# Kernel tuning notes

Hardware: AMD Instinct MI355X
Metric: run time of the kernel (lower is better)

## Reference

```python
import jax, jax.numpy as jnp
import numpy as np

N = 8192          # total genes
B = 16            # number of ragged batch groups (equal-size here: 512 each)
D = 768           # hidden_dim
NEG = -1.0e9      # mask fill value used by the original module


def setup_inputs() -> dict:
    key = jax.random.key(0)
    ks = jax.random.split(key, 10)
    s = 0.02
    inp = {
        "gene_embeddings": jax.random.normal(ks[0], (N, D), dtype=jnp.float32),
        # sorted group ids: 16 contiguous groups of 512 genes
        "batch": (jnp.arange(N) // (N // B)).astype(jnp.int64),
        "Wq": jax.random.normal(ks[1], (D, D), dtype=jnp.float32) * s,
        "bq": jnp.zeros((D,), dtype=jnp.float32),
        "Wk": jax.random.normal(ks[2], (D, D), dtype=jnp.float32) * s,
        "bk": jnp.zeros((D,), dtype=jnp.float32),
        "Wv": jax.random.normal(ks[3], (D, D), dtype=jnp.float32) * s,
        "bv": jnp.zeros((D,), dtype=jnp.float32),
        "Wo": jax.random.normal(ks[4], (D, D), dtype=jnp.float32) * s,
        "bo": jnp.zeros((D,), dtype=jnp.float32),
        "beta": jnp.ones((1,), dtype=jnp.float32) * 0.1,
    }
    return inp


def reference(gene_embeddings, batch, Wq, bq, Wk, bk, Wv, bv, Wo, bo, beta):
    # Single-head attention over full hidden_dim (num_heads unused in original).
    x = gene_embeddings
    q = x @ Wq.T + bq                      # [N, D]
    k = x @ Wk.T + bk
    v = x @ Wv.T + bv
    scale = 1.0 / jnp.sqrt(jnp.asarray(D, dtype=x.dtype))
    scores = (q @ k.T) * scale             # [N, N]
    # block-diagonal group mask + diagonal self-mask (same -1e9 fill as torch code)
    same_group = batch[:, None] == batch[None, :]
    eye = jnp.eye(N, dtype=bool)
    allow = same_group & (~eye)
    scores = jnp.where(allow, scores, NEG)
    weights = jax.nn.softmax(scores, axis=-1)   # dropout in eval mode -> identity
    dyn = weights @ v                       # [N, D]
    dyn = dyn @ Wo.T + bo
    return x + beta * dyn
```

## Files before the change

### kernel.cpp

```cpp
#include <hip/hip_runtime.h>
#include <hip/hip_bf16.h>
#include <cstdint>

using u16 = unsigned short;
using u32 = unsigned int;

typedef __bf16 bf16x8 __attribute__((ext_vector_type(8)));
typedef float  f32x4  __attribute__((ext_vector_type(4)));

__device__ __forceinline__ u32 f2b2(float a, float b) {
    __hip_bfloat162 h = __float22bfloat162_rn(float2{a, b});
    u32 u;
    __builtin_memcpy(&u, &h, 4);
    return u;
}
__device__ __forceinline__ float b2f(u16 b) {
    u32 u = (u32)b << 16;
    float f;
    __builtin_memcpy(&f, &u, 4);
    return f;
}

__device__ __forceinline__ void gload_lds16(const u16* g, u16* l) {
    __builtin_amdgcn_global_load_lds(
        (const __attribute__((address_space(1))) void*)g,
        (__attribute__((address_space(3))) void*)l,
        16, 0, 0);
}

__launch_bounds__(256)
__global__ void pack_kernel(const float* __restrict__ x,
                            const float* __restrict__ Wq,
                            const float* __restrict__ Wk,
                            const float* __restrict__ Wv,
                            const float* __restrict__ Wo,
                            const float* __restrict__ bq,
                            const float* __restrict__ bv,
                            const float* __restrict__ bo,
                            u16* __restrict__ xb,
                            u16* __restrict__ Wob,
                            u16* __restrict__ WqT,
                            u16* __restrict__ WkT,
                            u16* __restrict__ WvT,
                            float* __restrict__ czk,
                            float* __restrict__ bvoo)
{
    __shared__ u16 tl[64][72];
    const int b = blockIdx.x, tid = threadIdx.x;

    if (b < 3360) {
        int c = b * 256 + tid;
        long e = (long)c * 8;
        const float* src; u16* dst; long off;
        if (e < 6291456L) { src = x;  dst = xb;  off = e; }
        else              { src = Wo; dst = Wob; off = e - 6291456L; }
        float4 v0 = *(const float4*)(src + off);
        float4 v1 = *(const float4*)(src + off + 4);
        uint4 o;
        o.x = f2b2(v0.x, v0.y); o.y = f2b2(v0.z, v0.w);
        o.z = f2b2(v1.x, v1.y); o.w = f2b2(v1.z, v1.w);
        *(uint4*)(dst + off) = o;
    } else if (b < 3792) {
        int t = b - 3360;
        int w = t / 144, tt = t % 144;
        int tr = tt / 12, tc = tt % 12;
        const float* src0 = (w == 0) ? Wq : (w == 1) ? Wk : Wv;
        u16* dst0 = (w == 0) ? WqT : (w == 1) ? WkT : WvT;
        int lr = tid >> 2, lcb = (tid & 3) * 16;
        const float* src = src0 + (long)(tr * 64 + lr) * 768 + tc * 64 + lcb;
#pragma unroll
        for (int q = 0; q < 4; q++) {
            float4 v = *(const float4*)(src + q * 4);
            u32 p0 = f2b2(v.x, v.y), p1 = f2b2(v.z, v.w);
            tl[lr][lcb + q * 4 + 0] = (u16)p0;
            tl[lr][lcb + q * 4 + 1] = (u16)(p0 >> 16);
            tl[lr][lcb + q * 4 + 2] = (u16)p1;
            tl[lr][lcb + q * 4 + 3] = (u16)(p1 >> 16);
        }
        __syncthreads();
        int li = tid >> 2, lkb = (tid & 3) * 16;
        u16 o[16];
#pragma unroll
        for (int j = 0; j < 16; j++) o[j] = tl[lkb + j][li];
        u16* dst = dst0 + (long)(tc * 64 + li) * 768 + tr * 64 + lkb;
#pragma unroll
        for (int j = 0; j < 16; j++) dst[j] = o[j];
    } else if (b < 3984) {
        int wave = tid >> 6, lane = tid & 63;
        int j = (b - 3792) * 4 + wave;
        float acc = 0.f;
#pragma unroll
        for (int i = 0; i < 12; i++) {
            int rr = i * 64 + lane;
            acc += Wk[(long)rr * 768 + j] * bq[rr];
        }
#pragma unroll
        for (int d = 32; d; d >>= 1) acc += __shfl_xor(acc, d);
        if (lane == 0) czk[j] = acc;
    } else {
        int wave = tid >> 6, lane = tid & 63;
        int j = (b - 3984) * 4 + wave;
        float acc = 0.f;
#pragma unroll
        for (int i = 0; i < 12; i++) {
            int k = i * 64 + lane;
            acc += Wo[(long)j * 768 + k] * bv[k];
        }
#pragma unroll
        for (int d = 32; d; d >>= 1) acc += __shfl_xor(acc, d);
        if (lane == 0) bvoo[j] = acc + bo[j];
    }
}

template<int TM, int TN, int MODE>
__device__ __forceinline__ void gemm_body(
        const u16* __restrict__ A, int lda, long sAz,
        const u16* __restrict__ B, int ldb, long sBz,
        void* __restrict__ Cv, int ldc, long sCz,
        int K,
        const float* __restrict__ bias,
        float scale,
        u16* __restrict__ vTout)
{
    constexpr int FI = TM / 32;
    constexpr int FJ = TN / 32;
    constexpr int CA = TM / 64;
    constexpr int CB = TN / 64;

    __shared__ u16 As[2][TM * 32];
    __shared__ u16 Bs[2][TN * 32];

    const int tid  = threadIdx.x;
    const int g    = blockIdx.z;
    const u16* Ab = A + (long)g * sAz + (long)blockIdx.y * TM * lda;
    const u16* Bb = B + (long)g * sBz + (long)blockIdx.x * TN * ldb;

    const int wave = tid >> 6, lane = tid & 63;
    const int wm = (wave >> 1) * (TM / 2), wn = (wave & 1) * (TN / 2);
    const int ln15 = lane & 15, lq = lane >> 4;

    f32x4 acc[FI][FJ];
#pragma unroll
    for (int i = 0; i < FI; i++)
#pragma unroll
        for (int j = 0; j < FJ; j++)
            acc[i][j] = (f32x4){0.f, 0.f, 0.f, 0.f};

    const int srow = lane >> 2;
    const int sc   = ((lane & 3) ^ ((lane >> 4) & 3)) * 8;
    const u16* Ag[CA]; const u16* Bg[CB];
    int Al[CA], Bl[CB];
#pragma unroll
    for (int t = 0; t < CA; t++) {
        int c = wave * CA + t;
        Ag[t] = Ab + (long)(c * 16 + srow) * lda + sc;
        Al[t] = c * 512;
    }
#pragma unroll
    for (int t = 0; t < CB; t++) {
        int c = wave * CB + t;
        Bg[t] = Bb + (long)(c * 16 + srow) * ldb + sc;
        Bl[t] = c * 512;
    }

    const int foff = ln15 * 32 + ((lq ^ (ln15 >> 2)) * 8);
    const int nk = K >> 5;

#pragma unroll
    for (int t = 0; t < CA; t++) gload_lds16(Ag[t], &As[0][Al[t]]);
#pragma unroll
    for (int t = 0; t < CB; t++) gload_lds16(Bg[t], &Bs[0][Bl[t]]);

    for (int kt = 0; kt < nk; kt++) {
        const int cur = kt & 1;
        __syncthreads();
        if (kt + 1 < nk) {
            const int k0 = (kt + 1) * 32, nxt = cur ^ 1;
#pragma unroll
            for (int t = 0; t < CA; t++) gload_lds16(Ag[t] + k0, &As[nxt][Al[t]]);
#pragma unroll
            for (int t = 0; t < CB; t++) gload_lds16(Bg[t] + k0, &Bs[nxt][Bl[t]]);
        }

        bf16x8 af[FI], bfr[FJ];
#pragma unroll
        for (int i = 0; i < FI; i++)
            af[i] = *(const bf16x8*)&As[cur][(wm / 16 + i) * 512 + foff];
#pragma unroll
        for (int j = 0; j < FJ; j++)
            bfr[j] = *(const bf16x8*)&Bs[cur][(wn / 16 + j) * 512 + foff];
#pragma unroll
        for (int i = 0; i < FI; i++)
#pragma unroll
            for (int j = 0; j < FJ; j++)
                acc[i][j] = __builtin_amdgcn_mfma_f32_16x16x32_bf16(af[i], bfr[j], acc[i][j], 0, 0, 0);
    }

    const int baseRow = blockIdx.y * TM + wm;
    const int baseCol = blockIdx.x * TN + wn;

    if constexpr (MODE == 0) {
        if (baseCol < 768) {
            u16* C = (u16*)Cv;
#pragma unroll
            for (int i = 0; i < FI; i++)
#pragma unroll
                for (int j = 0; j < FJ; j++) {
                    int col = baseCol + j * 16 + ln15;
                    float bb = bias[col];
                    u32 p01 = f2b2(acc[i][j][0] + bb, acc[i][j][1] + bb);
                    u32 p23 = f2b2(acc[i][j][2] + bb, acc[i][j][3] + bb);
                    long r0 = (long)(baseRow + i * 16 + lq * 4) * ldc + col;
                    C[r0]           = (u16)p01;
                    C[r0 + ldc]     = (u16)(p01 >> 16);
                    C[r0 + 2 * ldc] = (u16)p23;
                    C[r0 + 3 * ldc] = (u16)(p23 >> 16);
                }
        } else {
#pragma unroll
            for (int i = 0; i < FI; i++)
#pragma unroll
                for (int j = 0; j < FJ; j++) {
                    int col = baseCol + j * 16 + ln15;
                    uint2 o;
                    o.x = f2b2(acc[i][j][0], acc[i][j][1]);
                    o.y = f2b2(acc[i][j][2], acc[i][j][3]);
                    *(uint2*)(vTout + (long)(col - 768) * 8192
                              + baseRow + i * 16 + lq * 4) = o;
                }
        }
    } else {
        u16* C = (u16*)Cv + (long)g * sCz;
#pragma unroll
        for (int i = 0; i < FI; i++)
#pragma unroll
            for (int j = 0; j < FJ; j++) {
                int col = baseCol + j * 16 + ln15;
                u32 p01 = f2b2(acc[i][j][0], acc[i][j][1]);
                u32 p23 = f2b2(acc[i][j][2], acc[i][j][3]);
                long r0 = (long)(baseRow + i * 16 + lq * 4) * ldc + col;
                C[r0]           = (u16)p01;
                C[r0 + ldc]     = (u16)(p01 >> 16);
                C[r0 + 2 * ldc] = (u16)p23;
                C[r0 + 3 * ldc] = (u16)(p23 >> 16);
            }
    }
}

__launch_bounds__(256)
__global__ void k_ww(const u16* WA, const u16* WB, void* WZplus)
{
    gemm_body<64, 128, 3>(WA, 768, 589824L, WB, 768, 589824L,
                          WZplus, 768, -589824L, 768,
                          nullptr, 0.f, nullptr);
}
__launch_bounds__(256)
__global__ void k_zv(const u16* A, const u16* B, void* C, const float* bias,
                     u16* vTout)
{
    gemm_body<128, 128, 0>(A, 768, 0, B, 768, 0, C, 768, 0, 768,
                           bias, 0.f, vTout);
}

__launch_bounds__(512)
__global__ void k_fattn(const u16* __restrict__ zbuf,
                        const u16* __restrict__ xb,
                        const u16* __restrict__ vwT,
                        float* __restrict__ out,
                        const float* __restrict__ bvoo,
                        const float* __restrict__ betaPtr,
                        float scale)
{
    __shared__ __align__(16) u16 smem[57344];
    u16* zl = smem;
    u16* xB = smem + 24576;
    u16* Pl = smem;
    u16* Vs = smem + 16384;

    const int rt = blockIdx.x, g = blockIdx.y;
    const int tid = threadIdx.x;
    const int wave = tid >> 6, lane = tid & 63;
    const int ln15 = lane & 15, lq = lane >> 4;
    const int srow = lane >> 2;
    const int sc   = ((lane & 3) ^ ((lane >> 4) & 3)) * 8;
    const int foff = ln15 * 32 + ((lq ^ (ln15 >> 2)) * 8);

    const long rowBase = (long)(g * 512 + rt * 32);
    const u16* Zb = zbuf + rowBase * 768;
    const u16* Xg = xb + (long)g * 512 * 768;

    const int wm = (wave >> 2) * 16;
    const int wn = (wave & 3) * 128;

#pragma unroll
    for (int n = 0; n < 6; n++) {
        int cc = n * 8 + wave;
        int zkt = cc >> 1, c = cc & 1;
        gload_lds16(Zb + (long)(c * 16 + srow) * 768 + zkt * 32 + sc,
                    &zl[cc * 512]);
    }
    const u16* Bg[4]; int Bl[4];
#pragma unroll
    for (int t = 0; t < 4; t++) {
        int c = wave * 4 + t;
        Bg[t] = Xg + (long)(c * 16 + srow) * 768 + sc;
        Bl[t] = c * 512;
    }
#pragma unroll
    for (int t = 0; t < 4; t++) gload_lds16(Bg[t], &xB[Bl[t]]);

    f32x4 acc[8];
#pragma unroll
    for (int j = 0; j < 8; j++) acc[j] = (f32x4){0.f, 0.f, 0.f, 0.f};

    for (int kt = 0; kt < 24; kt++) {
        const int cur = kt & 1;
        __syncthreads();
        if (kt + 1 < 24) {
            const int k0 = (kt + 1) * 32, nxt = cur ^ 1;
#pragma unroll
            for (int t = 0; t < 4; t++)
                gload_lds16(Bg[t] + k0, &xB[nxt * 16384 + Bl[t]]);
        }
        bf16x8 af = *(const bf16x8*)&zl[(kt * 2 + (wm >> 4)) * 512 + foff];
        bf16x8 bfr[8];
#pragma unroll
        for (int j = 0; j < 8; j++)
            bfr[j] = *(const bf16x8*)&xB[cur * 16384 + (wn / 16 + j) * 512 + foff];
#pragma unroll
        for (int j = 0; j < 8; j++)
            acc[j] = __builtin_amdgcn_mfma_f32_16x16x32_bf16(af, bfr[j], acc[j], 0, 0, 0);
    }

    __syncthreads();

#pragma unroll
    for (int sub = 0; sub < 2; sub++)
        gload_lds16(vwT + (long)(wave * 16 + srow) * 8192 + g * 512 + sub * 32 + sc,
                    &Vs[sub * 4096 + wave * 512]);

#pragma unroll
    for (int j = 0; j < 8; j++) {
        int col = wn + j * 16 + ln15;
        int c8 = col >> 3, b7 = col & 7;
#pragma unroll
        for (int r = 0; r < 4; r++) {
            int row = wm + lq * 4 + r;
            float v = acc[j][r] * scale;
            if (rt * 32 + row == col) v = -1.0e9f;
            Pl[(row * 64 + (c8 ^ (row & 7))) * 8 + b7] = (u16)f2b2(v, v);
        }
    }
    __syncthreads();

    {
        const int r = tid >> 4, seg = tid & 15;
        float e[32];
        float m = -3.0e38f;
#pragma unroll
        for (int q = 0; q < 4; q++) {
            int c8 = seg * 4 + q;
            uint4 qv = *(const uint4*)&Pl[(r * 64 + (c8 ^ (r & 7))) * 8];
            u32 w[4] = {qv.x, qv.y, qv.z, qv.w};
#pragma unroll
            for (int h = 0; h < 4; h++) {
                float lo = b2f((u16)w[h]);
                float hi = b2f((u16)(w[h] >> 16));
                e[q * 8 + h * 2]     = lo;
                e[q * 8 + h * 2 + 1] = hi;
                m = fmaxf(m, fmaxf(lo, hi));
            }
        }
        m = fmaxf(m, __shfl_xor(m, 1));
        m = fmaxf(m, __shfl_xor(m, 2));
        m = fmaxf(m, __shfl_xor(m, 4));
        m = fmaxf(m, __shfl_xor(m, 8));
        float sum = 0.f;
#pragma unroll
        for (int jj = 0; jj < 32; jj++) { e[jj] = __expf(e[jj] - m); sum += e[jj]; }
        sum += __shfl_xor(sum, 1);
        sum += __shfl_xor(sum, 2);
        sum += __shfl_xor(sum, 4);
        sum += __shfl_xor(sum, 8);
        const float inv = 1.0f / sum;
#pragma unroll
        for (int q = 0; q < 4; q++) {
            int c8 = seg * 4 + q;
            uint4 o;
            o.x = f2b2(e[q * 8 + 0] * inv, e[q * 8 + 1] * inv);
            o.y = f2b2(e[q * 8 + 2] * inv, e[q * 8 + 3] * inv);
            o.z = f2b2(e[q * 8 + 4] * inv, e[q * 8 + 5] * inv);
            o.w = f2b2(e[q * 8 + 6] * inv, e[q * 8 + 7] * inv);
            *(uint4*)&Pl[(r * 64 + (c8 ^ (r & 7))) * 8] = o;
        }
    }
    __syncthreads();

    const int wnP = (wave & 3) * 32;
    const int prow = wm + ln15;
    const float bet = betaPtr[0];

    bf16x8 apr[16];
#pragma unroll
    for (int k4 = 0; k4 < 16; k4++)
        apr[k4] = *(const bf16x8*)&Pl[(prow * 64 + ((k4 * 4 + lq) ^ (prow & 7))) * 8];

    f32x4 accP[2];
    accP[0] = (f32x4){0.f, 0.f, 0.f, 0.f};
    accP[1] = (f32x4){0.f, 0.f, 0.f, 0.f};

    for (int ct = 0; ct < 6; ct++) {
#pragma unroll
        for (int k8 = 0; k8 < 8; k8++) {
            const int t = ct * 8 + k8;
            const int cur = t & 1;
            __syncthreads();
            if (t + 1 < 48) {
                const int tn = t + 1, ctn = tn >> 3, kn = tn & 7;
#pragma unroll
                for (int sub = 0; sub < 2; sub++)
                    gload_lds16(vwT + (long)(ctn * 128 + wave * 16 + srow) * 8192
                                    + g * 512 + kn * 64 + sub * 32 + sc,
                                &Vs[(cur ^ 1) * 8192 + sub * 4096 + wave * 512]);
            }
#pragma unroll
            for (int sub = 0; sub < 2; sub++) {
                const int kt = k8 * 2 + sub;
                bf16x8 b0 = *(const bf16x8*)&Vs[cur * 8192 + sub * 4096
                                                + (wnP >> 4) * 512 + foff];
                bf16x8 b1 = *(const bf16x8*)&Vs[cur * 8192 + sub * 4096
                                                + ((wnP >> 4) + 1) * 512 + foff];
                accP[0] = __builtin_amdgcn_mfma_f32_16x16x32_bf16(apr[kt], b0, accP[0], 0, 0, 0);
                accP[1] = __builtin_amdgcn_mfma_f32_16x16x32_bf16(apr[kt], b1, accP[1], 0, 0, 0);
            }
        }
        {
            const u16* Xr = xb + (rowBase + wm + lq * 4) * 768;
            float* O = out + (rowBase + wm + lq * 4) * 768;
#pragma unroll
            for (int j = 0; j < 2; j++) {
                const int col = ct * 128 + wnP + j * 16 + ln15;
                const float bb = bvoo[col];
#pragma unroll
                for (int rr = 0; rr < 4; rr++)
                    O[rr * 768 + col] = b2f(Xr[rr * 768 + col])
                                        + bet * (accP[j][rr] + bb);
                accP[j] = (f32x4){0.f, 0.f, 0.f, 0.f};
            }
        }
    }
}

extern "C" void kernel_launch(void* const* d_in, const int* in_sizes, int n_in,
                              void* d_out, int out_size, void* d_ws, size_t ws_size,
                              hipStream_t stream)
{
    const float* x    = (const float*)d_in[0];
    const float* Wq   = (const float*)d_in[2];
    const float* bq   = (const float*)d_in[3];
    const float* Wk   = (const float*)d_in[4];
    const float* bk   = (const float*)d_in[5];
    const float* Wv   = (const float*)d_in[6];
    const float* bv   = (const float*)d_in[7];
    const float* Wo   = (const float*)d_in[8];
    const float* bo   = (const float*)d_in[9];
    const float* beta = (const float*)d_in[10];
    float* out = (float*)d_out;
    (void)bk;

    char* ws = (char*)d_ws;
    u16*   zbuf = (u16*)(ws + 0);
    u16*   vwT  = (u16*)(ws + 12582912);
    u16*   xb   = (u16*)(ws + 25165824);
    u16*   WA   = (u16*)(ws + 46137344);
    u16*   WB   = (u16*)(ws + 48496640);
    u16*   WZ   = (u16*)(ws + 50855936);
    float* czk  = (float*)(ws + 53215232);
    float* bvoo = (float*)(ws + 53218304);

    u16* Wob = WA;
    u16* WkT = WA + 589824;
    u16* WvT = WB;
    u16* WqT = WB + 589824;

    const float scale = 0.03608439182435161f;

    pack_kernel<<<4176, 256, 0, stream>>>(x, Wq, Wk, Wv, Wo, bq, bv, bo,
                                          xb, Wob, WqT, WkT, WvT, czk, bvoo);

    k_ww<<<dim3(6, 12, 2), 256, 0, stream>>>(WA, WB, (void*)(WZ + 589824L));

    k_zv<<<dim3(12, 64, 1), 256, 0, stream>>>(xb, WZ, (void*)zbuf, czk, vwT);

    k_fattn<<<dim3(16, 16), 512, 0, stream>>>(zbuf, xb, vwT, out, bvoo, beta,
                                              scale);
}
```

Before: 203.6 us.

## Restructure fused attention kernel with register-staged prefetch and in-register softmax

Rewrites the fused attention kernel's S=ZX^T stage so each wave owns a column strip, and prefetches the X tiles through registers several k-steps ahead instead of using async global-to-LDS loads with a barrier every step. Softmax now runs directly on the MFMA accumulators with cross-wave max/sum reductions through small LDS buffers. Normalisation is deferred to the output epilogue. The PV stage drops its per-step __syncthreads by giving each wave a private V slice in LDS, and blocks are remapped to a 1D grid with launch_bounds(512,2). These changes target barrier stalls and LDS round-trips, at the cost of more register pressure and a risk of LDS write/read hazards without barriers.

```diff
diff --git a/kernel.cpp b/kernel.cpp
--- a/kernel.cpp
+++ b/kernel.cpp
@@ -262,7 +262,7 @@
                            bias, 0.f, vTout);
 }
 
-__launch_bounds__(512)
+__launch_bounds__(512, 2)
 __global__ void k_fattn(const u16* __restrict__ zbuf,
                         const u16* __restrict__ xb,
                         const u16* __restrict__ vwT,
@@ -275,178 +275,251 @@
     u16* zl = smem;
     u16* xB = smem + 24576;
     u16* Pl = smem;
-    u16* Vs = smem + 16384;
-
-    const int rt = blockIdx.x, g = blockIdx.y;
+    float* redM = (float*)(smem + 16640);
+    float* redS = (float*)(smem + 16640 + 512);
+    u16* Vs = smem + 24576;
+
+    const int bx = blockIdx.x;
+    const int lg = ((bx & 7) << 5) + (bx >> 3);
+    const int g = lg >> 4, rt = lg & 15;
+
     const int tid = threadIdx.x;
     const int wave = tid >> 6, lane = tid & 63;
     const int ln15 = lane & 15, lq = lane >> 4;
     const int srow = lane >> 2;
-    const int sc   = ((lane & 3) ^ ((lane >> 4) & 3)) * 8;
+    const int sc = ((lane & 3) ^ ((lane >> 4) & 3)) * 8;
     const int foff = ln15 * 32 + ((lq ^ (ln15 >> 2)) * 8);
 
     const long rowBase = (long)(g * 512 + rt * 32);
     const u16* Zb = zbuf + rowBase * 768;
     const u16* Xg = xb + (long)g * 512 * 768;
 
-    const int wm = (wave >> 2) * 16;
-    const int wn = (wave & 3) * 128;
-
 #pragma unroll
     for (int n = 0; n < 6; n++) {
         int cc = n * 8 + wave;
-        int zkt = cc >> 1, c = cc & 1;
-        gload_lds16(Zb + (long)(c * 16 + srow) * 768 + zkt * 32 + sc,
+        gload_lds16(Zb + (long)((cc & 1) * 16 + srow) * 768 + (cc >> 1) * 32 + sc,
                     &zl[cc * 512]);
     }
-    const u16* Bg[4]; int Bl[4];
+    const u16* xsrc[4];
+    u16* xd[4];
 #pragma unroll
     for (int t = 0; t < 4; t++) {
-        int c = wave * 4 + t;
-        Bg[t] = Xg + (long)(c * 16 + srow) * 768 + sc;
-        Bl[t] = c * 512;
-    }
-#pragma unroll
-    for (int t = 0; t < 4; t++) gload_lds16(Bg[t], &xB[Bl[t]]);
-
-    f32x4 acc[8];
-#pragma unroll
-    for (int j = 0; j < 8; j++) acc[j] = (f32x4){0.f, 0.f, 0.f, 0.f};
-
-    for (int kt = 0; kt < 24; kt++) {
-        const int cur = kt & 1;
-        __syncthreads();
-        if (kt + 1 < 24) {
-            const int k0 = (kt + 1) * 32, nxt = cur ^ 1;
-#pragma unroll
-            for (int t = 0; t < 4; t++)
-                gload_lds16(Bg[t] + k0, &xB[nxt * 16384 + Bl[t]]);
-        }
-        bf16x8 af = *(const bf16x8*)&zl[(kt * 2 + (wm >> 4)) * 512 + foff];
-        bf16x8 bfr[8];
-#pragma unroll
-        for (int j = 0; j < 8; j++)
-            bfr[j] = *(const bf16x8*)&xB[cur * 16384 + (wn / 16 + j) * 512 + foff];
-#pragma unroll
-        for (int j = 0; j < 8; j++)
-            acc[j] = __builtin_amdgcn_mfma_f32_16x16x32_bf16(af, bfr[j], acc[j], 0, 0, 0);
-    }
-
+        xsrc[t] = Xg + (long)((wave * 4 + t) * 16 + srow) * 768 + sc;
+        xd[t] = xB + (wave * 4 + t) * 512 + lane * 8;
+    }
+    uint4 vrA[4], vrB[4];
+#pragma unroll
+    for (int t = 0; t < 4; t++) vrA[t] = *(const uint4*)(xsrc[t]);
+#pragma unroll
+    for (int t = 0; t < 4; t++) *(uint4*)(xd[t]) = vrA[t];
+#pragma unroll
+    for (int t = 0; t < 4; t++) vrA[t] = *(const uint4*)(xsrc[t] + 32);
+#pragma unroll
+    for (int t = 0; t < 4; t++) vrB[t] = *(const uint4*)(xsrc[t] + 64);
     __syncthreads();
 
-#pragma unroll
-    for (int sub = 0; sub < 2; sub++)
-        gload_lds16(vwT + (long)(wave * 16 + srow) * 8192 + g * 512 + sub * 32 + sc,
-                    &Vs[sub * 4096 + wave * 512]);
-
-#pragma unroll
-    for (int j = 0; j < 8; j++) {
-        int col = wn + j * 16 + ln15;
-        int c8 = col >> 3, b7 = col & 7;
-#pragma unroll
-        for (int r = 0; r < 4; r++) {
-            int row = wm + lq * 4 + r;
-            float v = acc[j][r] * scale;
-            if (rt * 32 + row == col) v = -1.0e9f;
-            Pl[(row * 64 + (c8 ^ (row & 7))) * 8 + b7] = (u16)f2b2(v, v);
-        }
+    f32x4 acc0[4], acc1[4];
+#pragma unroll
+    for (int j = 0; j < 4; j++) {
+        acc0[j] = (f32x4){0.f, 0.f, 0.f, 0.f};
+        acc1[j] = (f32x4){0.f, 0.f, 0.f, 0.f};
+    }
+
+    for (int kt2 = 0; kt2 < 12; kt2++) {
+        const int ke = kt2 * 2;
+        {
+#pragma unroll
+            for (int t = 0; t < 4; t++) *(uint4*)(xd[t] + 16384) = vrA[t];
+            int kl = ke + 3; if (kl > 23) kl = 23;
+#pragma unroll
+            for (int t = 0; t < 4; t++) vrA[t] = *(const uint4*)(xsrc[t] + kl * 32);
+            bf16x8 af0 = *(const bf16x8*)&zl[(ke * 2 + 0) * 512 + foff];
+            bf16x8 af1 = *(const bf16x8*)&zl[(ke * 2 + 1) * 512 + foff];
+#pragma unroll
+            for (int j = 0; j < 4; j++) {
+                bf16x8 bfr = *(const bf16x8*)&xB[(wave * 4 + j) * 512 + foff];
+                acc0[j] = __builtin_amdgcn_mfma_f32_16x16x32_bf16(af0, bfr, acc0[j], 0, 0, 0);
+                acc1[j] = __builtin_amdgcn_mfma_f32_16x16x32_bf16(af1, bfr, acc1[j], 0, 0, 0);
+            }
+        }
+        {
+            const int ko = ke + 1;
+#pragma unroll
+            for (int t = 0; t < 4; t++) *(uint4*)(xd[t]) = vrB[t];
+            int kl = ko + 3; if (kl > 23) kl = 23;
+#pragma unroll
+            for (int t = 0; t < 4; t++) vrB[t] = *(const uint4*)(xsrc[t] + kl * 32);
+            bf16x8 af0 = *(const bf16x8*)&zl[(ko * 2 + 0) * 512 + foff];
+            bf16x8 af1 = *(const bf16x8*)&zl[(ko * 2 + 1) * 512 + foff];
+#pragma unroll
+            for (int j = 0; j < 4; j++) {
+                bf16x8 bfr = *(const bf16x8*)&xB[16384 + (wave * 4 + j) * 512 + foff];
+                acc0[j] = __builtin_amdgcn_mfma_f32_16x16x32_bf16(af0, bfr, acc0[j], 0, 0, 0);
+                acc1[j] = __builtin_amdgcn_mfma_f32_16x16x32_bf16(af1, bfr, acc1[j], 0, 0, 0);
+            }
+        }
+    }
+
+    const int wm3 = (wave >> 2) * 16;
+    const int wn3 = (wave & 3) * 32;
+    const u16* vbase[4];
+    u16* vdst[4];
+#pragma unroll
+    for (int scj = 0; scj < 4; scj++) {
+        vbase[scj] = vwT + (long)(wn3 + (scj & 1) * 16 + srow) * 8192
+                     + g * 512 + (scj >> 1) * 32 + sc;
+        vdst[scj] = Vs + wave * 2048 + scj * 512 + lane * 8;
+    }
+    uint4 w0[4], w1[4];
+#pragma unroll
+    for (int scj = 0; scj < 4; scj++) {
+        w0[scj] = *(const uint4*)(vbase[scj]);
+        w1[scj] = *(const uint4*)(vbase[scj] + 64);
     }
     __syncthreads();
 
-    {
-        const int r = tid >> 4, seg = tid & 15;
-        float e[32];
-        float m = -3.0e38f;
-#pragma unroll
-        for (int q = 0; q < 4; q++) {
-            int c8 = seg * 4 + q;
-            uint4 qv = *(const uint4*)&Pl[(r * 64 + (c8 ^ (r & 7))) * 8];
-            u32 w[4] = {qv.x, qv.y, qv.z, qv.w};
-#pragma unroll
-            for (int h = 0; h < 4; h++) {
-                float lo = b2f((u16)w[h]);
-                float hi = b2f((u16)(w[h] >> 16));
-                e[q * 8 + h * 2]     = lo;
-                e[q * 8 + h * 2 + 1] = hi;
-                m = fmaxf(m, fmaxf(lo, hi));
-            }
-        }
-        m = fmaxf(m, __shfl_xor(m, 1));
-        m = fmaxf(m, __shfl_xor(m, 2));
-        m = fmaxf(m, __shfl_xor(m, 4));
-        m = fmaxf(m, __shfl_xor(m, 8));
-        float sum = 0.f;
-#pragma unroll
-        for (int jj = 0; jj < 32; jj++) { e[jj] = __expf(e[jj] - m); sum += e[jj]; }
-        sum += __shfl_xor(sum, 1);
-        sum += __shfl_xor(sum, 2);
-        sum += __shfl_xor(sum, 4);
-        sum += __shfl_xor(sum, 8);
-        const float inv = 1.0f / sum;
-#pragma unroll
-        for (int q = 0; q < 4; q++) {
-            int c8 = seg * 4 + q;
-            uint4 o;
-            o.x = f2b2(e[q * 8 + 0] * inv, e[q * 8 + 1] * inv);
-            o.y = f2b2(e[q * 8 + 2] * inv, e[q * 8 + 3] * inv);
-            o.z = f2b2(e[q * 8 + 4] * inv, e[q * 8 + 5] * inv);
-            o.w = f2b2(e[q * 8 + 6] * inv, e[q * 8 + 7] * inv);
-            *(uint4*)&Pl[(r * 64 + (c8 ^ (r & 7))) * 8] = o;
+    float e0[4][4], e1[4][4], mx0[4], mx1[4];
+#pragma unroll
+    for (int rr = 0; rr < 4; rr++) { mx0[rr] = -3.0e38f; mx1[rr] = -3.0e38f; }
+#pragma unroll
+    for (int j = 0; j < 4; j++)
+#pragma unroll
+        for (int rr = 0; rr < 4; rr++) {
+            const int col = wave * 64 + j * 16 + ln15;
+            float v0 = acc0[j][rr] * scale;
+            float v1 = acc1[j][rr] * scale;
+            if (rt * 32 + lq * 4 + rr == col) v0 = -1.0e9f;
+            if (rt * 32 + 16 + lq * 4 + rr == col) v1 = -1.0e9f;
+            e0[j][rr] = v0; e1[j][rr] = v1;
+            mx0[rr] = fmaxf(mx0[rr], v0);
+            mx1[rr] = fmaxf(mx1[rr], v1);
+        }
+#pragma unroll
+    for (int rr = 0; rr < 4; rr++)
+#pragma unroll
+        for (int d = 1; d < 16; d <<= 1) {
+            mx0[rr] = fmaxf(mx0[rr], __shfl_xor(mx0[rr], d));
+            mx1[rr] = fmaxf(mx1[rr], __shfl_xor(mx1[rr], d));
+        }
+    if (ln15 == 0) {
+#pragma unroll
+        for (int rr = 0; rr < 4; rr++) {
+            redM[(lq * 4 + rr) * 8 + wave] = mx0[rr];
+            redM[(16 + lq * 4 + rr) * 8 + wave] = mx1[rr];
         }
     }
     __syncthreads();
-
-    const int wnP = (wave & 3) * 32;
-    const int prow = wm + ln15;
+    float m0[4], m1[4], s0[4], s1[4];
+#pragma unroll
+    for (int rr = 0; rr < 4; rr++) {
+        float a = -3.0e38f, b = -3.0e38f;
+#pragma unroll
+        for (int w = 0; w < 8; w++) {
+            a = fmaxf(a, redM[(lq * 4 + rr) * 8 + w]);
+            b = fmaxf(b, redM[(16 + lq * 4 + rr) * 8 + w]);
+        }
+        m0[rr] = a; m1[rr] = b; s0[rr] = 0.f; s1[rr] = 0.f;
+    }
+#pragma unroll
+    for (int j = 0; j < 4; j++)
+#pragma unroll
+        for (int rr = 0; rr < 4; rr++) {
+            e0[j][rr] = __expf(e0[j][rr] - m0[rr]); s0[rr] += e0[j][rr];
+            e1[j][rr] = __expf(e1[j][rr] - m1[rr]); s1[rr] += e1[j][rr];
+        }
+#pragma unroll
+    for (int rr = 0; rr < 4; rr++)
+#pragma unroll
+        for (int d = 1; d < 16; d <<= 1) {
+            s0[rr] += __shfl_xor(s0[rr], d);
+            s1[rr] += __shfl_xor(s1[rr], d);
+        }
+    if (ln15 == 0) {
+#pragma unroll
+        for (int rr = 0; rr < 4; rr++) {
+            redS[(lq * 4 + rr) * 8 + wave] = s0[rr];
+            redS[(16 + lq * 4 + rr) * 8 + wave] = s1[rr];
+        }
+    }
+#pragma unroll
+    for (int j = 0; j < 4; j++)
+#pragma unroll
+        for (int rr = 0; rr < 4; rr++) {
+            const int col = wave * 64 + j * 16 + ln15;
+            Pl[(lq * 4 + rr) * 520 + col] = (u16)f2b2(e0[j][rr], e0[j][rr]);
+            Pl[(16 + lq * 4 + rr) * 520 + col] = (u16)f2b2(e1[j][rr], e1[j][rr]);
+        }
+    __syncthreads();
+
+    float invS[4];
+#pragma unroll
+    for (int rr = 0; rr < 4; rr++) {
+        float s = 0.f;
+#pragma unroll
+        for (int w = 0; w < 8; w++) s += redS[(wm3 + lq * 4 + rr) * 8 + w];
+        invS[rr] = 1.0f / s;
+    }
+    bf16x8 apr[16];
+#pragma unroll
+    for (int k4 = 0; k4 < 16; k4++)
+        apr[k4] = *(const bf16x8*)&Pl[(wm3 + ln15) * 520 + (k4 * 4 + lq) * 8];
+
     const float bet = betaPtr[0];
-
-    bf16x8 apr[16];
-#pragma unroll
-    for (int k4 = 0; k4 < 16; k4++)
-        apr[k4] = *(const bf16x8*)&Pl[(prow * 64 + ((k4 * 4 + lq) ^ (prow & 7))) * 8];
-
-    f32x4 accP[2];
-    accP[0] = (f32x4){0.f, 0.f, 0.f, 0.f};
-    accP[1] = (f32x4){0.f, 0.f, 0.f, 0.f};
+    f32x4 aP0 = (f32x4){0.f, 0.f, 0.f, 0.f};
+    f32x4 aP1 = (f32x4){0.f, 0.f, 0.f, 0.f};
 
     for (int ct = 0; ct < 6; ct++) {
 #pragma unroll
         for (int k8 = 0; k8 < 8; k8++) {
             const int t = ct * 8 + k8;
-            const int cur = t & 1;
-            __syncthreads();
-            if (t + 1 < 48) {
-                const int tn = t + 1, ctn = tn >> 3, kn = tn & 7;
-#pragma unroll
-                for (int sub = 0; sub < 2; sub++)
-                    gload_lds16(vwT + (long)(ctn * 128 + wave * 16 + srow) * 8192
-                                    + g * 512 + kn * 64 + sub * 32 + sc,
-                                &Vs[(cur ^ 1) * 8192 + sub * 4096 + wave * 512]);
+            if ((k8 & 1) == 0) {
+#pragma unroll
+                for (int scj = 0; scj < 4; scj++) *(uint4*)(vdst[scj]) = w0[scj];
+                int tt = t + 2; if (tt > 47) tt = 47;
+                const long off = (long)(tt >> 3) * 1048576 + (tt & 7) * 64;
+#pragma unroll
+                for (int scj = 0; scj < 4; scj++)
+                    w0[scj] = *(const uint4*)(vbase[scj] + off);
+            } else {
+#pragma unroll
+                for (int scj = 0; scj < 4; scj++) *(uint4*)(vdst[scj]) = w1[scj];
+                int tt = t + 2; if (tt > 47) tt = 47;
+                const long off = (long)(tt >> 3) * 1048576 + (tt & 7) * 64;
+#pragma unroll
+                for (int scj = 0; scj < 4; scj++)
+                    w1[scj] = *(const uint4*)(vbase[scj] + off);
             }
-#pragma unroll
-            for (int sub = 0; sub < 2; sub++) {
-                const int kt = k8 * 2 + sub;
-                bf16x8 b0 = *(const bf16x8*)&Vs[cur * 8192 + sub * 4096
-                                                + (wnP >> 4) * 512 + foff];
-                bf16x8 b1 = *(const bf16x8*)&Vs[cur * 8192 + sub * 4096
-                                                + ((wnP >> 4) + 1) * 512 + foff];
-                accP[0] = __builtin_amdgcn_mfma_f32_16x16x32_bf16(apr[kt], b0, accP[0], 0, 0, 0);
-                accP[1] = __builtin_amdgcn_mfma_f32_16x16x32_bf16(apr[kt], b1, accP[1], 0, 0, 0);
-            }
+            __builtin_amdgcn_sched_barrier(0);
+            bf16x8 b00 = *(const bf16x8*)&Vs[wave * 2048 + 0 * 512 + foff];
+            bf16x8 b01 = *(const bf16x8*)&Vs[wave * 2048 + 1 * 512 + foff];
+            bf16x8 b10 = *(const bf16x8*)&Vs[wave * 2048 + 2 * 512 + foff];
+            bf16x8 b11 = *(const bf16x8*)&Vs[wave * 2048 + 3 * 512 + foff];
+            aP0 = __builtin_amdgcn_mfma_f32_16x16x32_bf16(apr[k8 * 2 + 0], b00, aP0, 0, 0, 0);
+            aP1 = __builtin_amdgcn_mfma_f32_16x16x32_bf16(apr[k8 * 2 + 0], b01, aP1, 0, 0, 0);
+            aP0 = __builtin_amdgcn_mfma_f32_16x16x32_bf16(apr[k8 * 2 + 1], b10, aP0, 0, 0, 0);
+            aP1 = __builtin_amdgcn_mfma_f32_16x16x32_bf16(apr[k8 * 2 + 1], b11, aP1, 0, 0, 0);
         }
         {
-            const u16* Xr = xb + (rowBase + wm + lq * 4) * 768;
-            float* O = out + (rowBase + wm + lq * 4) * 768;
-#pragma unroll
-            for (int j = 0; j < 2; j++) {
-                const int col = ct * 128 + wnP + j * 16 + ln15;
+            const u16* Xr = xb + (rowBase + wm3 + lq * 4) * 768;
+            float* O = out + (rowBase + wm3 + lq * 4) * 768;
+            {
+                const int col = ct * 128 + wn3 + ln15;
                 const float bb = bvoo[col];
 #pragma unroll
                 for (int rr = 0; rr < 4; rr++)
                     O[rr * 768 + col] = b2f(Xr[rr * 768 + col])
-                                        + bet * (accP[j][rr] + bb);
-                accP[j] = (f32x4){0.f, 0.f, 0.f, 0.f};
+                                        + bet * (invS[rr] * aP0[rr] + bb);
             }
+            {
+                const int col = ct * 128 + wn3 + 16 + ln15;
+                const float bb = bvoo[col];
+#pragma unroll
+                for (int rr = 0; rr < 4; rr++)
+                    O[rr * 768 + col] = b2f(Xr[rr * 768 + col])
+                                        + bet * (invS[rr] * aP1[rr] + bb);
+            }
+            aP0 = (f32x4){0.f, 0.f, 0.f, 0.f};
+            aP1 = (f32x4){0.f, 0.f, 0.f, 0.f};
         }
     }
 }
@@ -492,6 +565,6 @@
 
     k_zv<<<dim3(12, 64, 1), 256, 0, stream>>>(xb, WZ, (void*)zbuf, czk, vwT);
 
-    k_fattn<<<dim3(16, 16), 512, 0, stream>>>(zbuf, xb, vwT, out, bvoo, beta,
-                                              scale);
-}
+    k_fattn<<<dim3(256), 512, 0, stream>>>(zbuf, xb, vwT, out, bvoo, beta,
+                                           scale);
+}
```

Result: slower. 301.1 us (+47.9%).

## Compute softmax in registers with cross-wave LDS reduction, deferred normalization, larger V tiles

Applied to the files above, without the earlier changes.

Softmax max and sum are now computed directly on the MFMA accumulators, with shuffles and a small LDS reduction across waves. This removes the separate pass that round-tripped bf16 scores through LDS, and the 1/sum scaling is applied in the output epilogue. The V streaming loop now loads 128-column K chunks, which halves the number of barrier-separated pipeline steps. The grid is flattened to 1D with a swizzled block-to-group mapping, which may change L2 locality. The unnormalized probabilities are rounded to bf16 before normalization, a slight numeric change.

```diff
diff --git a/kernel.cpp b/kernel.cpp
--- a/kernel.cpp
+++ b/kernel.cpp
@@ -275,14 +275,19 @@
     u16* zl = smem;
     u16* xB = smem + 24576;
     u16* Pl = smem;
-    u16* Vs = smem + 16384;
-
-    const int rt = blockIdx.x, g = blockIdx.y;
+    float* redM = (float*)(smem + 16384);
+    float* redS = (float*)(smem + 16640);
+    u16* Vs = smem + 18432;
+
+    const int bx = blockIdx.x;
+    const int lg = ((bx & 7) << 5) + (bx >> 3);
+    const int g = lg >> 4, rt = lg & 15;
+
     const int tid = threadIdx.x;
     const int wave = tid >> 6, lane = tid & 63;
     const int ln15 = lane & 15, lq = lane >> 4;
     const int srow = lane >> 2;
-    const int sc   = ((lane & 3) ^ ((lane >> 4) & 3)) * 8;
+    const int sc = ((lane & 3) ^ ((lane >> 4) & 3)) * 8;
     const int foff = ln15 * 32 + ((lq ^ (ln15 >> 2)) * 8);
 
     const long rowBase = (long)(g * 512 + rt * 32);
@@ -295,8 +300,7 @@
 #pragma unroll
     for (int n = 0; n < 6; n++) {
         int cc = n * 8 + wave;
-        int zkt = cc >> 1, c = cc & 1;
-        gload_lds16(Zb + (long)(c * 16 + srow) * 768 + zkt * 32 + sc,
+        gload_lds16(Zb + (long)((cc & 1) * 16 + srow) * 768 + (cc >> 1) * 32 + sc,
                     &zl[cc * 512]);
     }
     const u16* Bg[4]; int Bl[4];
@@ -335,118 +339,140 @@
     __syncthreads();
 
 #pragma unroll
-    for (int sub = 0; sub < 2; sub++)
+    for (int sub = 0; sub < 4; sub++)
         gload_lds16(vwT + (long)(wave * 16 + srow) * 8192 + g * 512 + sub * 32 + sc,
                     &Vs[sub * 4096 + wave * 512]);
 
+    float mx[4];
+#pragma unroll
+    for (int rr = 0; rr < 4; rr++) mx[rr] = -3.0e38f;
+#pragma unroll
+    for (int j = 0; j < 8; j++)
+#pragma unroll
+        for (int rr = 0; rr < 4; rr++) {
+            const int col = wn + j * 16 + ln15;
+            float v = acc[j][rr] * scale;
+            if (rt * 32 + wm + lq * 4 + rr == col) v = -1.0e9f;
+            acc[j][rr] = v;
+            mx[rr] = fmaxf(mx[rr], v);
+        }
+#pragma unroll
+    for (int rr = 0; rr < 4; rr++) {
+        mx[rr] = fmaxf(mx[rr], __shfl_xor(mx[rr], 1));
+        mx[rr] = fmaxf(mx[rr], __shfl_xor(mx[rr], 2));
+        mx[rr] = fmaxf(mx[rr], __shfl_xor(mx[rr], 4));
+        mx[rr] = fmaxf(mx[rr], __shfl_xor(mx[rr], 8));
+    }
+    if (ln15 == 0) {
+#pragma unroll
+        for (int rr = 0; rr < 4; rr++)
+            redM[(wm + lq * 4 + rr) * 4 + (wave & 3)] = mx[rr];
+    }
+    __syncthreads();
+
+    float m[4], s[4];
+#pragma unroll
+    for (int rr = 0; rr < 4; rr++) {
+        float4 rm = *(const float4*)&redM[(wm + lq * 4 + rr) * 4];
+        m[rr] = fmaxf(fmaxf(rm.x, rm.y), fmaxf(rm.z, rm.w));
+        s[rr] = 0.f;
+    }
+#pragma unroll
+    for (int j = 0; j < 8; j++)
+#pragma unroll
+        for (int rr = 0; rr < 4; rr++) {
+            float p = __expf(acc[j][rr] - m[rr]);
+            acc[j][rr] = p;
+            s[rr] += p;
+        }
+#pragma unroll
+    for (int rr = 0; rr < 4; rr++) {
+        s[rr] += __shfl_xor(s[rr], 1);
+        s[rr] += __shfl_xor(s[rr], 2);
+        s[rr] += __shfl_xor(s[rr], 4);
+        s[rr] += __shfl_xor(s[rr], 8);
+    }
+    if (ln15 == 0) {
+#pragma unroll
+        for (int rr = 0; rr < 4; rr++)
+            redS[(wm + lq * 4 + rr) * 4 + (wave & 3)] = s[rr];
+    }
 #pragma unroll
     for (int j = 0; j < 8; j++) {
-        int col = wn + j * 16 + ln15;
-        int c8 = col >> 3, b7 = col & 7;
-#pragma unroll
-        for (int r = 0; r < 4; r++) {
-            int row = wm + lq * 4 + r;
-            float v = acc[j][r] * scale;
-            if (rt * 32 + row == col) v = -1.0e9f;
-            Pl[(row * 64 + (c8 ^ (row & 7))) * 8 + b7] = (u16)f2b2(v, v);
+        const int col = wn + j * 16 + ln15;
+        const int c8 = col >> 3, b7 = col & 7;
+#pragma unroll
+        for (int rr = 0; rr < 4; rr++) {
+            const int row = wm + lq * 4 + rr;
+            Pl[(row * 64 + (c8 ^ (row & 7))) * 8 + b7] = (u16)f2b2(acc[j][rr], acc[j][rr]);
         }
     }
     __syncthreads();
 
-    {
-        const int r = tid >> 4, seg = tid & 15;
-        float e[32];
-        float m = -3.0e38f;
-#pragma unroll
-        for (int q = 0; q < 4; q++) {
-            int c8 = seg * 4 + q;
-            uint4 qv = *(const uint4*)&Pl[(r * 64 + (c8 ^ (r & 7))) * 8];
-            u32 w[4] = {qv.x, qv.y, qv.z, qv.w};
-#pragma unroll
-            for (int h = 0; h < 4; h++) {
-                float lo = b2f((u16)w[h]);
-                float hi = b2f((u16)(w[h] >> 16));
-                e[q * 8 + h * 2]     = lo;
-                e[q * 8 + h * 2 + 1] = hi;
-                m = fmaxf(m, fmaxf(lo, hi));
-            }
-        }
-        m = fmaxf(m, __shfl_xor(m, 1));
-        m = fmaxf(m, __shfl_xor(m, 2));
-        m = fmaxf(m, __shfl_xor(m, 4));
-        m = fmaxf(m, __shfl_xor(m, 8));
-        float sum = 0.f;
-#pragma unroll
-        for (int jj = 0; jj < 32; jj++) { e[jj] = __expf(e[jj] - m); sum += e[jj]; }
-        sum += __shfl_xor(sum, 1);
-        sum += __shfl_xor(sum, 2);
-        sum += __shfl_xor(sum, 4);
-        sum += __shfl_xor(sum, 8);
-        const float inv = 1.0f / sum;
-#pragma unroll
-        for (int q = 0; q < 4; q++) {
-            int c8 = seg * 4 + q;
-            uint4 o;
-            o.x = f2b2(e[q * 8 + 0] * inv, e[q * 8 + 1] * inv);
-            o.y = f2b2(e[q * 8 + 2] * inv, e[q * 8 + 3] * inv);
-            o.z = f2b2(e[q * 8 + 4] * inv, e[q * 8 + 5] * inv);
-            o.w = f2b2(e[q * 8 + 6] * inv, e[q * 8 + 7] * inv);
-            *(uint4*)&Pl[(r * 64 + (c8 ^ (r & 7))) * 8] = o;
-        }
-    }
-    __syncthreads();
-
-    const int wnP = (wave & 3) * 32;
+    float invS[4];
+#pragma unroll
+    for (int rr = 0; rr < 4; rr++) {
+        float4 rs = *(const float4*)&redS[(wm + lq * 4 + rr) * 4];
+        invS[rr] = 1.0f / (rs.x + rs.y + rs.z + rs.w);
+    }
+
     const int prow = wm + ln15;
-    const float bet = betaPtr[0];
-
     bf16x8 apr[16];
 #pragma unroll
     for (int k4 = 0; k4 < 16; k4++)
         apr[k4] = *(const bf16x8*)&Pl[(prow * 64 + ((k4 * 4 + lq) ^ (prow & 7))) * 8];
 
-    f32x4 accP[2];
-    accP[0] = (f32x4){0.f, 0.f, 0.f, 0.f};
-    accP[1] = (f32x4){0.f, 0.f, 0.f, 0.f};
+    const int wnP = (wave & 3) * 32;
+    const float bet = betaPtr[0];
+    f32x4 aP0 = (f32x4){0.f, 0.f, 0.f, 0.f};
+    f32x4 aP1 = (f32x4){0.f, 0.f, 0.f, 0.f};
 
     for (int ct = 0; ct < 6; ct++) {
 #pragma unroll
-        for (int k8 = 0; k8 < 8; k8++) {
-            const int t = ct * 8 + k8;
-            const int cur = t & 1;
+        for (int kn2 = 0; kn2 < 4; kn2++) {
+            const int ts = ct * 4 + kn2;
+            const int cur = ts & 1;
             __syncthreads();
-            if (t + 1 < 48) {
-                const int tn = t + 1, ctn = tn >> 3, kn = tn & 7;
-#pragma unroll
-                for (int sub = 0; sub < 2; sub++)
+            if (ts + 1 < 24) {
+                const int tn = ts + 1, ctn = tn >> 2, kn = tn & 3;
+                const int nxt = cur ^ 1;
+#pragma unroll
+                for (int sub = 0; sub < 4; sub++)
                     gload_lds16(vwT + (long)(ctn * 128 + wave * 16 + srow) * 8192
-                                    + g * 512 + kn * 64 + sub * 32 + sc,
-                                &Vs[(cur ^ 1) * 8192 + sub * 4096 + wave * 512]);
+                                    + g * 512 + kn * 128 + sub * 32 + sc,
+                                &Vs[nxt * 16384 + sub * 4096 + wave * 512]);
             }
 #pragma unroll
-            for (int sub = 0; sub < 2; sub++) {
-                const int kt = k8 * 2 + sub;
-                bf16x8 b0 = *(const bf16x8*)&Vs[cur * 8192 + sub * 4096
+            for (int sub = 0; sub < 4; sub++) {
+                bf16x8 b0 = *(const bf16x8*)&Vs[cur * 16384 + sub * 4096
                                                 + (wnP >> 4) * 512 + foff];
-                bf16x8 b1 = *(const bf16x8*)&Vs[cur * 8192 + sub * 4096
+                bf16x8 b1 = *(const bf16x8*)&Vs[cur * 16384 + sub * 4096
                                                 + ((wnP >> 4) + 1) * 512 + foff];
-                accP[0] = __builtin_amdgcn_mfma_f32_16x16x32_bf16(apr[kt], b0, accP[0], 0, 0, 0);
-                accP[1] = __builtin_amdgcn_mfma_f32_16x16x32_bf16(apr[kt], b1, accP[1], 0, 0, 0);
+                aP0 = __builtin_amdgcn_mfma_f32_16x16x32_bf16(apr[kn2 * 4 + sub], b0, aP0, 0, 0, 0);
+                aP1 = __builtin_amdgcn_mfma_f32_16x16x32_bf16(apr[kn2 * 4 + sub], b1, aP1, 0, 0, 0);
             }
         }
         {
             const u16* Xr = xb + (rowBase + wm + lq * 4) * 768;
             float* O = out + (rowBase + wm + lq * 4) * 768;
-#pragma unroll
-            for (int j = 0; j < 2; j++) {
-                const int col = ct * 128 + wnP + j * 16 + ln15;
+            {
+                const int col = ct * 128 + wnP + ln15;
                 const float bb = bvoo[col];
 #pragma unroll
                 for (int rr = 0; rr < 4; rr++)
                     O[rr * 768 + col] = b2f(Xr[rr * 768 + col])
-                                        + bet * (accP[j][rr] + bb);
-                accP[j] = (f32x4){0.f, 0.f, 0.f, 0.f};
+                                        + bet * (invS[rr] * aP0[rr] + bb);
             }
+            {
+                const int col = ct * 128 + wnP + 16 + ln15;
+                const float bb = bvoo[col];
+#pragma unroll
+                for (int rr = 0; rr < 4; rr++)
+                    O[rr * 768 + col] = b2f(Xr[rr * 768 + col])
+                                        + bet * (invS[rr] * aP1[rr] + bb);
+            }
+            aP0 = (f32x4){0.f, 0.f, 0.f, 0.f};
+            aP1 = (f32x4){0.f, 0.f, 0.f, 0.f};
         }
     }
 }
@@ -492,6 +518,6 @@
 
     k_zv<<<dim3(12, 64, 1), 256, 0, stream>>>(xb, WZ, (void*)zbuf, czk, vwT);
 
-    k_fattn<<<dim3(16, 16), 512, 0, stream>>>(zbuf, xb, vwT, out, bvoo, beta,
-                                              scale);
-}
+    k_fattn<<<dim3(256), 512, 0, stream>>>(zbuf, xb, vwT, out, bvoo, beta,
+                                           scale);
+}
```

Measured after the change: 193.9 us. 4.8% less time.
